# Performance work log

Measured on AMD Instinct MI355X. Metric: run time of the kernel, lower is better.

The kernel has to match this reference:

```python
import jax, jax.numpy as jnp
import numpy as np

B, L, C, S, D = 2, 64, 256, 256, 512

def setup_inputs() -> dict:
    key = jax.random.key(0)
    ks = jax.random.split(key, 6)
    scale = 1.0 / np.sqrt(D)
    return {
        "queries": jax.random.normal(ks[0], (B, L, C, D), dtype=jnp.float32),
        "keys": jax.random.normal(ks[1], (B, L, S, D), dtype=jnp.float32),
        "values": jax.random.normal(ks[2], (B, L, S, D), dtype=jnp.float32),
        "Wq": jax.random.normal(ks[3], (D, D), dtype=jnp.float32) * scale,
        "bq": jnp.zeros((D,), dtype=jnp.float32),
        "Wkv": jax.random.normal(ks[4], (D, D), dtype=jnp.float32) * scale,
        "bkv": jnp.zeros((D,), dtype=jnp.float32),
        "Wo": jax.random.normal(ks[5], (D, D), dtype=jnp.float32) * scale,
        "bo": jnp.zeros((D,), dtype=jnp.float32),
    }

def reference(queries, keys, values, Wq, bq, Wkv, bkv, Wo, bo):
    d = queries.shape[-1]
    scale = 1.0 / jnp.sqrt(jnp.asarray(d, queries.dtype))
    # linear projections (torch Linear: x @ W.T + b); kv_projection shared for K and V
    q = queries @ Wq.T + bq            # [B, L, C, D]
    k = keys @ Wkv.T + bkv             # [B, L, S, D]
    v = values @ Wkv.T + bkv           # [B, L, S, D]
    scores = jnp.einsum('blcd,blsd->blcs', q, k)
    attn = jax.nn.softmax(scale * scores, axis=-1)  # dropout is identity in eval
    out = jnp.einsum('blcs,blsd->blcd', attn, v)
    return out @ Wo.T + bo
```

## Files before the change

kernel.cpp:

```cpp
#include <hip/hip_runtime.h>
#include <hip/hip_fp16.h>
#include <stdint.h>


typedef _Float16 f16;
typedef __attribute__((ext_vector_type(8))) _Float16 f16x8;
typedef __attribute__((ext_vector_type(4))) _Float16 f16x4;
typedef __attribute__((ext_vector_type(4))) float f32x4;

#define BM 128
#define BN 128
#define BK 64

__device__ __forceinline__ void glds16(const void* g, void* l)
{
    __builtin_amdgcn_global_load_lds(
        (const __attribute__((address_space(1))) void*)(uintptr_t)g,
        (__attribute__((address_space(3))) void*)(uint32_t)(uintptr_t)l,
        16, 0, 0);
}

template<bool A_F32, bool OUT_F32, bool TRANS_OUT, bool BIAS>
__global__ __launch_bounds__(256)
void gemm_nt(const void* __restrict__ Ap, const f16* __restrict__ Btp,
             const float* __restrict__ bias, void* __restrict__ Cp,
             int M, int N, int K, long sA, long sB, long sC)
{
    __shared__ f16 As[BM][BK];
    __shared__ f16 Bs[BN][BK];

    const int z    = blockIdx.z;
    const int m0   = blockIdx.y * BM;
    const int n0   = blockIdx.x * BN;
    const int tid  = threadIdx.x;
    const int lane = tid & 63;
    const int wave = tid >> 6;
    const int quad = lane >> 4;
    const int l16  = lane & 15;
    const int wr   = wave >> 1;
    const int wc   = wave & 1;

    const float* Af = (const float*)Ap + (long)z * sA;
    const f16*   Ah = (const f16*)Ap + (long)z * sA;
    const f16*   Bt = Btp + (long)z * sB;

    f32x4 acc[4][4];
    #pragma unroll
    for (int i = 0; i < 4; ++i)
        #pragma unroll
        for (int j = 0; j < 4; ++j)
            acc[i][j] = (f32x4){0.f, 0.f, 0.f, 0.f};

    const int i8 = lane >> 3;
    const int cl = (((lane & 7) - i8) & 7) * 8;

    const int ar = tid >> 3;
    const int ac = (tid & 7) * 8;

    float4 pre[8];
    auto load_a_f32 = [&](int k0) {
        #pragma unroll
        for (int h = 0; h < 4; ++h) {
            const float* p = Af + (long)(m0 + h * 32 + ar) * K + k0 + ac;
            pre[2 * h]     = *(const float4*)p;
            pre[2 * h + 1] = *(const float4*)(p + 4);
        }
    };
    auto store_a = [&]() {
        #pragma unroll
        for (int h = 0; h < 4; ++h) {
            const int r  = h * 32 + ar;
            const int pc = (ac + ((r & 7) * 8)) & 63;
            f16x8 v;
            v[0] = (f16)pre[2*h].x;   v[1] = (f16)pre[2*h].y;
            v[2] = (f16)pre[2*h].z;   v[3] = (f16)pre[2*h].w;
            v[4] = (f16)pre[2*h+1].x; v[5] = (f16)pre[2*h+1].y;
            v[6] = (f16)pre[2*h+1].z; v[7] = (f16)pre[2*h+1].w;
            *(f16x8*)&As[r][pc] = v;
        }
    };

    for (int k0 = 0; k0 < K; k0 += BK) {
        if (A_F32) {
            if (k0 == 0) load_a_f32(0);
            if (k0) __syncthreads();
            #pragma unroll
            for (int j = 0; j < 4; ++j) {
                const int R0 = (wave * 4 + j) * 8;
                glds16(Bt + (long)(n0 + R0 + i8) * K + k0 + cl, &Bs[R0][0]);
            }
            store_a();
        } else {
            if (k0) __syncthreads();
            #pragma unroll
            for (int j = 0; j < 4; ++j) {
                const int R0 = (wave * 4 + j) * 8;
                glds16(Ah + (long)(m0 + R0 + i8) * K + k0 + cl, &As[R0][0]);
                glds16(Bt + (long)(n0 + R0 + i8) * K + k0 + cl, &Bs[R0][0]);
            }
        }
        __syncthreads();
        if (A_F32 && k0 + BK < K) load_a_f32(k0 + BK);

        #pragma unroll
        for (int ksub = 0; ksub < 2; ++ksub) {
            f16x8 af[4], bf[4];
            #pragma unroll
            for (int i = 0; i < 4; ++i) {
                const int r  = wr * 64 + i * 16 + l16;
                const int pc = ((ksub * 32 + quad * 8) + ((r & 7) * 8)) & 63;
                af[i] = *(const f16x8*)&As[r][pc];
            }
            #pragma unroll
            for (int j = 0; j < 4; ++j) {
                const int r  = wc * 64 + j * 16 + l16;
                const int pc = ((ksub * 32 + quad * 8) + ((r & 7) * 8)) & 63;
                bf[j] = *(const f16x8*)&Bs[r][pc];
            }
            #pragma unroll
            for (int i = 0; i < 4; ++i)
                #pragma unroll
                for (int j = 0; j < 4; ++j)
                    acc[i][j] = __builtin_amdgcn_mfma_f32_16x16x32_f16(
                        af[i], bf[j], acc[i][j], 0, 0, 0);
        }
    }

    #pragma unroll
    for (int i = 0; i < 4; ++i) {
        #pragma unroll
        for (int j = 0; j < 4; ++j) {
            const int col = n0 + wc * 64 + j * 16 + l16;
            const float bv = BIAS ? bias[col] : 0.0f;
            #pragma unroll
            for (int r = 0; r < 4; ++r) {
                const int row = m0 + wr * 64 + i * 16 + quad * 4 + r;
                const float val = acc[i][j][r] + bv;
                if (TRANS_OUT) {
                    ((f16*)Cp)[(long)(row >> 8) * 131072 + (long)col * 256 + (row & 255)] = (f16)val;
                } else if (OUT_F32) {
                    ((float*)Cp)[(long)z * sC + (long)row * N + col] = val;
                } else {
                    ((f16*)Cp)[(long)z * sC + (long)row * N + col] = (f16)val;
                }
            }
        }
    }
}

__global__ __launch_bounds__(256)
void softmax_rows(const float* __restrict__ S, f16* __restrict__ P)
{
    const int row  = blockIdx.x * 4 + (threadIdx.x >> 6);
    const int lane = threadIdx.x & 63;
    const float scale = 0.044194173824159216f;
    const float4 v = *(const float4*)(S + (long)row * 256 + lane * 4);
    const float a0 = v.x * scale, a1 = v.y * scale, a2 = v.z * scale, a3 = v.w * scale;
    float m = fmaxf(fmaxf(a0, a1), fmaxf(a2, a3));
    #pragma unroll
    for (int off = 32; off > 0; off >>= 1) m = fmaxf(m, __shfl_xor(m, off, 64));
    const float e0 = __expf(a0 - m), e1 = __expf(a1 - m), e2 = __expf(a2 - m), e3 = __expf(a3 - m);
    float s = e0 + e1 + e2 + e3;
    #pragma unroll
    for (int off = 32; off > 0; off >>= 1) s += __shfl_xor(s, off, 64);
    const float inv = 1.0f / s;
    f16x4 o;
    o[0] = (f16)(e0 * inv); o[1] = (f16)(e1 * inv);
    o[2] = (f16)(e2 * inv); o[3] = (f16)(e3 * inv);
    *(f16x4*)&P[(long)row * 256 + lane * 4] = o;
}

__global__ __launch_bounds__(256)
void cvt3(const float* __restrict__ a, const float* __restrict__ b,
          const float* __restrict__ c, f16* __restrict__ oa,
          f16* __restrict__ ob, f16* __restrict__ oc)
{
    const int w = blockIdx.x >> 8;
    const int t = ((blockIdx.x & 255) * 256 + threadIdx.x) * 4;
    const float* src = (w == 0) ? a : (w == 1) ? b : c;
    f16* dst = (w == 0) ? oa : (w == 1) ? ob : oc;
    const float4 v = *(const float4*)(src + t);
    f16x4 o;
    o[0] = (f16)v.x; o[1] = (f16)v.y; o[2] = (f16)v.z; o[3] = (f16)v.w;
    *(f16x4*)(dst + t) = o;
}

extern "C" void kernel_launch(void* const* d_in, const int* in_sizes, int n_in,
                              void* d_out, int out_size, void* d_ws, size_t ws_size,
                              hipStream_t stream)
{
    const float* queries = (const float*)d_in[0];
    const float* keys    = (const float*)d_in[1];
    const float* values  = (const float*)d_in[2];
    const float* Wq      = (const float*)d_in[3];
    const float* bq      = (const float*)d_in[4];
    const float* Wkv     = (const float*)d_in[5];
    const float* bkv     = (const float*)d_in[6];
    const float* Wo      = (const float*)d_in[7];
    const float* bo      = (const float*)d_in[8];
    float* out = (float*)d_out;

    f16* ws  = (f16*)d_ws;
    f16* wq  = ws;
    f16* wkv = ws + 262144;
    f16* wo  = ws + 524288;
    f16* qh  = ws + 786432;
    f16* kh  = qh + 16777216;
    f16* vT  = kh + 16777216;
    float* scores = (float*)(vT + 16777216);
    f16* P  = qh;
    f16* ao = (f16*)scores;

    cvt3<<<768, 256, 0, stream>>>(Wq, Wkv, Wo, wq, wkv, wo);

    const dim3 blk(256);
    gemm_nt<true,  false, false, true><<<dim3(4, 256, 1), blk, 0, stream>>>(
        queries, wq,  bq,  qh, 32768, 512, 512, 0, 0, 0);
    gemm_nt<true,  false, false, true><<<dim3(4, 256, 1), blk, 0, stream>>>(
        keys,    wkv, bkv, kh, 32768, 512, 512, 0, 0, 0);
    gemm_nt<true,  false, true,  true><<<dim3(4, 256, 1), blk, 0, stream>>>(
        values,  wkv, bkv, vT, 32768, 512, 512, 0, 0, 0);
    gemm_nt<false, true,  false, false><<<dim3(2, 2, 128), blk, 0, stream>>>(
        qh, kh, nullptr, scores, 256, 256, 512, 131072, 131072, 65536);
    softmax_rows<<<8192, 256, 0, stream>>>(scores, P);
    gemm_nt<false, false, false, false><<<dim3(4, 2, 128), blk, 0, stream>>>(
        P, vT, nullptr, ao, 256, 512, 256, 65536, 131072, 131072);
    gemm_nt<false, true,  false, true><<<dim3(4, 256, 1), blk, 0, stream>>>(
        ao, wo, bo, out, 32768, 512, 512, 0, 0, 0);
}
```

Baseline: 402.2 us.

## Fuse QK^T GEMM with row softmax and add XCD-aware block swizzle

Replaces the separate QK^T GEMM (fp32 score output) and softmax kernel with one 512-thread kernel. Each block computes a 128x256 score tile, reduces row max and sum through shared memory, and writes fp16 probabilities directly, so the fp32 score matrix no longer goes to and from global memory. All GEMMs also switch to a 1D grid whose block-index mapping groups tiles by XCD, aiming for better L2 locality. The trade-offs are a larger shared-memory footprint and fewer, bigger blocks (256) for the fused kernel, which may cut occupancy.

```diff
diff --git a/kernel.cpp b/kernel.cpp
--- a/kernel.cpp
+++ b/kernel.cpp
@@ -20,18 +20,30 @@
         16, 0, 0);
 }
 
-template<bool A_F32, bool OUT_F32, bool TRANS_OUT, bool BIAS>
+template<bool A_F32, bool OUT_F32, bool TRANS_OUT, bool BIAS, int SWZ>
 __global__ __launch_bounds__(256)
 void gemm_nt(const void* __restrict__ Ap, const f16* __restrict__ Btp,
              const float* __restrict__ bias, void* __restrict__ Cp,
-             int M, int N, int K, long sA, long sB, long sC)
+             int N, int K, long sA, long sB, long sC)
 {
     __shared__ f16 As[BM][BK];
     __shared__ f16 Bs[BN][BK];
 
-    const int z    = blockIdx.z;
-    const int m0   = blockIdx.y * BM;
-    const int n0   = blockIdx.x * BN;
+    const int p    = blockIdx.x;
+    const int xcd  = p & 7;
+    const int slot = p >> 3;
+    int z, m0, n0;
+    if (SWZ == 1) {
+        z  = 0;
+        m0 = (xcd + 8 * (slot >> 2)) * BM;
+        n0 = (slot & 3) * BN;
+    } else {
+        z  = xcd + 8 * (slot >> 3);
+        const int inner = slot & 7;
+        m0 = (inner >> 2) * BM;
+        n0 = (inner & 3) * BN;
+    }
+
     const int tid  = threadIdx.x;
     const int lane = tid & 63;
     const int wave = tid >> 6;
@@ -61,9 +73,9 @@
     auto load_a_f32 = [&](int k0) {
         #pragma unroll
         for (int h = 0; h < 4; ++h) {
-            const float* p = Af + (long)(m0 + h * 32 + ar) * K + k0 + ac;
-            pre[2 * h]     = *(const float4*)p;
-            pre[2 * h + 1] = *(const float4*)(p + 4);
+            const float* s = Af + (long)(m0 + h * 32 + ar) * K + k0 + ac;
+            pre[2 * h]     = *(const float4*)s;
+            pre[2 * h + 1] = *(const float4*)(s + 4);
         }
     };
     auto store_a = [&]() {
@@ -148,26 +160,150 @@
     }
 }
 
-__global__ __launch_bounds__(256)
-void softmax_rows(const float* __restrict__ S, f16* __restrict__ P)
-{
-    const int row  = blockIdx.x * 4 + (threadIdx.x >> 6);
-    const int lane = threadIdx.x & 63;
+__global__ __launch_bounds__(512)
+void qk_softmax(const f16* __restrict__ q, const f16* __restrict__ k,
+                f16* __restrict__ P)
+{
+    __shared__ f16 As[128][64];
+    __shared__ f16 Bs[256][64];
+    __shared__ float red[2][128][4];
+
+    const int p    = blockIdx.x;
+    const int xcd  = p & 7;
+    const int slot = p >> 3;
+    const int z    = xcd + 8 * (slot >> 1);
+    const int m0   = (slot & 1) * 128;
+
+    const int tid  = threadIdx.x;
+    const int lane = tid & 63;
+    const int wave = tid >> 6;
+    const int quad = lane >> 4;
+    const int l16  = lane & 15;
+    const int wr   = wave >> 2;
+    const int wc   = wave & 3;
+
+    const f16* Aq = q + (long)z * 131072 + (long)m0 * 512;
+    const f16* Bk = k + (long)z * 131072;
+
+    f32x4 acc[4][4];
+    #pragma unroll
+    for (int i = 0; i < 4; ++i)
+        #pragma unroll
+        for (int j = 0; j < 4; ++j)
+            acc[i][j] = (f32x4){0.f, 0.f, 0.f, 0.f};
+
+    const int i8 = lane >> 3;
+    const int cl = (((lane & 7) - i8) & 7) * 8;
+
+    for (int k0 = 0; k0 < 512; k0 += BK) {
+        if (k0) __syncthreads();
+        #pragma unroll
+        for (int g = 0; g < 2; ++g) {
+            const int R0 = (wave * 2 + g) * 8;
+            glds16(Aq + (long)(R0 + i8) * 512 + k0 + cl, &As[R0][0]);
+        }
+        #pragma unroll
+        for (int g = 0; g < 4; ++g) {
+            const int R0 = (wave * 4 + g) * 8;
+            glds16(Bk + (long)(R0 + i8) * 512 + k0 + cl, &Bs[R0][0]);
+        }
+        __syncthreads();
+
+        #pragma unroll
+        for (int ksub = 0; ksub < 2; ++ksub) {
+            f16x8 af[4], bf[4];
+            #pragma unroll
+            for (int i = 0; i < 4; ++i) {
+                const int r  = wr * 64 + i * 16 + l16;
+                const int pc = ((ksub * 32 + quad * 8) + ((r & 7) * 8)) & 63;
+                af[i] = *(const f16x8*)&As[r][pc];
+            }
+            #pragma unroll
+            for (int j = 0; j < 4; ++j) {
+                const int r  = wc * 64 + j * 16 + l16;
+                const int pc = ((ksub * 32 + quad * 8) + ((r & 7) * 8)) & 63;
+                bf[j] = *(const f16x8*)&Bs[r][pc];
+            }
+            #pragma unroll
+            for (int i = 0; i < 4; ++i)
+                #pragma unroll
+                for (int j = 0; j < 4; ++j)
+                    acc[i][j] = __builtin_amdgcn_mfma_f32_16x16x32_f16(
+                        af[i], bf[j], acc[i][j], 0, 0, 0);
+        }
+    }
+
     const float scale = 0.044194173824159216f;
-    const float4 v = *(const float4*)(S + (long)row * 256 + lane * 4);
-    const float a0 = v.x * scale, a1 = v.y * scale, a2 = v.z * scale, a3 = v.w * scale;
-    float m = fmaxf(fmaxf(a0, a1), fmaxf(a2, a3));
-    #pragma unroll
-    for (int off = 32; off > 0; off >>= 1) m = fmaxf(m, __shfl_xor(m, off, 64));
-    const float e0 = __expf(a0 - m), e1 = __expf(a1 - m), e2 = __expf(a2 - m), e3 = __expf(a3 - m);
-    float s = e0 + e1 + e2 + e3;
-    #pragma unroll
-    for (int off = 32; off > 0; off >>= 1) s += __shfl_xor(s, off, 64);
-    const float inv = 1.0f / s;
-    f16x4 o;
-    o[0] = (f16)(e0 * inv); o[1] = (f16)(e1 * inv);
-    o[2] = (f16)(e2 * inv); o[3] = (f16)(e3 * inv);
-    *(f16x4*)&P[(long)row * 256 + lane * 4] = o;
+    float st[4][4];
+    #pragma unroll
+    for (int i = 0; i < 4; ++i)
+        #pragma unroll
+        for (int r = 0; r < 4; ++r) {
+            float m = acc[i][0][r];
+            #pragma unroll
+            for (int j = 1; j < 4; ++j) m = fmaxf(m, acc[i][j][r]);
+            st[i][r] = m;
+        }
+    #pragma unroll
+    for (int off = 1; off < 16; off <<= 1)
+        #pragma unroll
+        for (int i = 0; i < 4; ++i)
+            #pragma unroll
+            for (int r = 0; r < 4; ++r)
+                st[i][r] = fmaxf(st[i][r], __shfl_xor(st[i][r], off, 64));
+    if (l16 == 0)
+        #pragma unroll
+        for (int i = 0; i < 4; ++i)
+            #pragma unroll
+            for (int r = 0; r < 4; ++r)
+                red[0][wr * 64 + i * 16 + quad * 4 + r][wc] = st[i][r];
+    __syncthreads();
+
+    #pragma unroll
+    for (int i = 0; i < 4; ++i)
+        #pragma unroll
+        for (int r = 0; r < 4; ++r) {
+            const int row = wr * 64 + i * 16 + quad * 4 + r;
+            const float m = fmaxf(fmaxf(red[0][row][0], red[0][row][1]),
+                                  fmaxf(red[0][row][2], red[0][row][3]));
+            float s = 0.f;
+            #pragma unroll
+            for (int j = 0; j < 4; ++j) {
+                const float e = __expf(scale * (acc[i][j][r] - m));
+                acc[i][j][r] = e;
+                s += e;
+            }
+            st[i][r] = s;
+        }
+    #pragma unroll
+    for (int off = 1; off < 16; off <<= 1)
+        #pragma unroll
+        for (int i = 0; i < 4; ++i)
+            #pragma unroll
+            for (int r = 0; r < 4; ++r)
+                st[i][r] += __shfl_xor(st[i][r], off, 64);
+    if (l16 == 0)
+        #pragma unroll
+        for (int i = 0; i < 4; ++i)
+            #pragma unroll
+            for (int r = 0; r < 4; ++r)
+                red[1][wr * 64 + i * 16 + quad * 4 + r][wc] = st[i][r];
+    __syncthreads();
+
+    #pragma unroll
+    for (int i = 0; i < 4; ++i)
+        #pragma unroll
+        for (int r = 0; r < 4; ++r) {
+            const int row = wr * 64 + i * 16 + quad * 4 + r;
+            const float inv = 1.0f / (red[1][row][0] + red[1][row][1] +
+                                      red[1][row][2] + red[1][row][3]);
+            #pragma unroll
+            for (int j = 0; j < 4; ++j) {
+                const int col = wc * 64 + j * 16 + l16;
+                P[(long)z * 65536 + (long)(m0 + row) * 256 + col] =
+                    (f16)(acc[i][j][r] * inv);
+            }
+        }
 }
 
 __global__ __launch_bounds__(256)
@@ -207,24 +343,21 @@
     f16* qh  = ws + 786432;
     f16* kh  = qh + 16777216;
     f16* vT  = kh + 16777216;
-    float* scores = (float*)(vT + 16777216);
-    f16* P  = qh;
-    f16* ao = (f16*)scores;
+    f16* P   = vT + 16777216;
+    f16* ao  = kh;
 
     cvt3<<<768, 256, 0, stream>>>(Wq, Wkv, Wo, wq, wkv, wo);
 
     const dim3 blk(256);
-    gemm_nt<true,  false, false, true><<<dim3(4, 256, 1), blk, 0, stream>>>(
-        queries, wq,  bq,  qh, 32768, 512, 512, 0, 0, 0);
-    gemm_nt<true,  false, false, true><<<dim3(4, 256, 1), blk, 0, stream>>>(
-        keys,    wkv, bkv, kh, 32768, 512, 512, 0, 0, 0);
-    gemm_nt<true,  false, true,  true><<<dim3(4, 256, 1), blk, 0, stream>>>(
-        values,  wkv, bkv, vT, 32768, 512, 512, 0, 0, 0);
-    gemm_nt<false, true,  false, false><<<dim3(2, 2, 128), blk, 0, stream>>>(
-        qh, kh, nullptr, scores, 256, 256, 512, 131072, 131072, 65536);
-    softmax_rows<<<8192, 256, 0, stream>>>(scores, P);
-    gemm_nt<false, false, false, false><<<dim3(4, 2, 128), blk, 0, stream>>>(
-        P, vT, nullptr, ao, 256, 512, 256, 65536, 131072, 131072);
-    gemm_nt<false, true,  false, true><<<dim3(4, 256, 1), blk, 0, stream>>>(
-        ao, wo, bo, out, 32768, 512, 512, 0, 0, 0);
-}
+    gemm_nt<true,  false, false, true, 1><<<1024, blk, 0, stream>>>(
+        queries, wq,  bq,  qh, 512, 512, 0, 0, 0);
+    gemm_nt<true,  false, false, true, 1><<<1024, blk, 0, stream>>>(
+        keys,    wkv, bkv, kh, 512, 512, 0, 0, 0);
+    gemm_nt<true,  false, true,  true, 1><<<1024, blk, 0, stream>>>(
+        values,  wkv, bkv, vT, 512, 512, 0, 0, 0);
+    qk_softmax<<<256, 512, 0, stream>>>(qh, kh, P);
+    gemm_nt<false, false, false, false, 2><<<1024, blk, 0, stream>>>(
+        P, vT, nullptr, ao, 512, 256, 65536, 131072, 131072);
+    gemm_nt<false, true,  false, true, 1><<<1024, blk, 0, stream>>>(
+        ao, wo, bo, out, 512, 512, 0, 0, 0);
+}
```

New measurement: 370.8 us. 1.08x faster.
